# Kernel optimization log

Hardware: AMD Instinct MI355X
Metric: run time of the kernel (lower is better)

Reference implementation:

```python
import jax, jax.numpy as jnp
import numpy as np

ORB = 54          # unify_orb_num = 27 * 2
N_ATOMS = 64
N_EDGES = 1536
N_P = 256
N_Q = 384
F_P, F_Q, F_O = 0.0002, 0.0001, 0.00015


def setup_inputs() -> dict:
    key = jax.random.key(0)
    ks = jax.random.split(key, 16)
    M = ORB * N_ATOMS
    lattice_vector = 10.0 * jnp.eye(3, dtype=jnp.float32) + 0.1 * jax.random.normal(ks[0], (3, 3), jnp.float32)
    atoms_positions = 10.0 * jax.random.uniform(ks[1], (N_ATOMS, 3), jnp.float32)
    edge_src = jax.random.randint(ks[2], (N_EDGES,), 0, N_ATOMS, jnp.int32)
    edge_dst = jax.random.randint(ks[3], (N_EDGES,), 0, N_ATOMS, jnp.int32)
    # edge_vec = (pos_j - pos_i) + R @ lattice so that round(cell_inv @ R_dis) recovers integer R
    R_int = jax.random.randint(ks[4], (N_EDGES, 3), -2, 3).astype(jnp.float32)
    edge_vec = (atoms_positions[edge_dst] - atoms_positions[edge_src]) + R_int @ lattice_vector
    hr_gt = jax.random.normal(ks[5], (N_EDGES, ORB, ORB), jnp.float32)
    hr_pred = hr_gt + 0.1 * jax.random.normal(ks[6], (N_EDGES, ORB, ORB), jnp.float32)
    kpt_coord = jax.random.uniform(ks[7], (3,), jnp.float32)
    s = np.float32(1.0 / np.sqrt(M))
    P_re = s * jax.random.normal(ks[8], (N_P, M), jnp.float32)
    P_im = s * jax.random.normal(ks[9], (N_P, M), jnp.float32)
    Q_re = s * jax.random.normal(ks[10], (N_Q, M), jnp.float32)
    Q_im = s * jax.random.normal(ks[11], (N_Q, M), jnp.float32)
    H_gt = jax.random.normal(ks[12], (N_EDGES, ORB, ORB), jnp.float32)
    pred_H = H_gt + 0.1 * jax.random.normal(ks[13], (N_EDGES, ORB, ORB), jnp.float32)
    overlap = jax.random.normal(ks[14], (N_EDGES, ORB, ORB), jnp.float32)
    mask_tensor = jnp.ones((N_EDGES, ORB, ORB), jnp.float32)
    return dict(edge_vec=edge_vec, lattice_vector=lattice_vector, atoms_positions=atoms_positions,
                hr_gt=hr_gt, hr_pred=hr_pred, kpt_coord=kpt_coord,
                P_re=P_re, P_im=P_im, Q_re=Q_re, Q_im=Q_im,
                H_gt=H_gt, pred_H=pred_H, overlap=overlap, mask_tensor=mask_tensor,
                edge_src=edge_src, edge_dst=edge_dst)


def _forward(edge_vec, lattice_vector, atoms_positions, hr_gt, hr_pred, kpt_coord,
             P_re, P_im, Q_re, Q_im, H_gt, pred_H, overlap, mask_tensor,
             edge_src, edge_dst):
    M = ORB * atoms_positions.shape[0]
    # --- get_R_list (vectorized): R_tot = round(inv(L^T) @ (edge_vec - (pos_j - pos_i))) ---
    cell_inv = jnp.linalg.inv(lattice_vector.T)
    R_dis = edge_vec - (atoms_positions[edge_dst] - atoms_positions[edge_src])   # [E,3]
    R_tot = jnp.round(R_dis @ cell_inv.T)                                        # [E,3]
    # --- cal_wfc_hk_vectorized: phase factors + block scatter into dense hk ---
    phase = jnp.exp(2j * jnp.pi * (R_tot @ kpt_coord)).astype(jnp.complex64)     # [E]
    idx = jnp.arange(ORB)
    rows = edge_src[:, None, None].astype(jnp.int32) * ORB + idx[None, :, None]  # [E,ORB,1]
    cols = edge_dst[:, None, None].astype(jnp.int32) * ORB + idx[None, None, :]  # [E,1,ORB]
    flat = (rows * M + cols).reshape(-1)                                         # [E*ORB*ORB]

    def build_hk(hr):
        contrib = phase[:, None, None] * hr.astype(jnp.complex64)                # [E,ORB,ORB]
        return jnp.zeros((M * M,), jnp.complex64).at[flat].add(contrib.reshape(-1)).reshape(M, M)

    P = (P_re + 1j * P_im).astype(jnp.complex64)   # [N_P, M]
    Q = (Q_re + 1j * Q_im).astype(jnp.complex64)   # [N_Q, M]

    def project(hk):
        PcH = P.conj() @ hk                        # [N_P, M]
        QcH = Q.conj() @ hk                        # [N_Q, M]
        return PcH @ P.T, QcH @ Q.T, PcH @ Q.T     # [N_P,N_P], [N_Q,N_Q], [N_P,N_Q]

    rP1, rQ1, rPQ1 = project(build_hk(hr_gt))
    rP2, rQ2, rPQ2 = project(build_hk(hr_pred))

    # --- grep_min_mu ---
    f_R = 1.0 - F_P - F_Q - F_O
    N1 = jnp.sum(mask_tensor)
    N2 = N_P * N_P
    N3 = N_Q * N_Q
    N4 = N_P * N_Q
    n1 = f_R * jnp.sum((pred_H - H_gt) * overlap) / N1   # real inputs: real(sum(x*conj(s)))
    d1 = f_R * jnp.sum(overlap * overlap) / N1
    n2 = F_P * jnp.real(jnp.trace(rP2 - rP1)) / N2
    d2 = F_P / N_P
    n3 = F_Q * jnp.real(jnp.trace(rQ2 - rQ1)) / N3
    d3 = F_Q / N_Q
    mu = jax.lax.stop_gradient((n1 + n2 + n3) / (d1 + d2 + d3))  # torch float(mu) detaches

    # --- cal_loss: L1 terms (reduction='none' then sum) ---
    l1 = lambda a, b: jnp.abs(a - b)
    loss_hr = l1(H_gt + mu * overlap, pred_H).sum()
    eyeP = jnp.eye(N_P, dtype=jnp.float32)
    eyeQ = jnp.eye(N_Q, dtype=jnp.float32)
    loss_p = l1(jnp.real(rP1) + mu * eyeP, jnp.real(rP2)).sum() + l1(jnp.imag(rP1), jnp.imag(rP2)).sum()
    loss_q = l1(jnp.real(rQ1) + mu * eyeQ, jnp.real(rQ2)).sum() + l1(jnp.imag(rQ1), jnp.imag(rQ2)).sum()
    loss_pq = l1(jnp.real(rPQ1), jnp.real(rPQ2)).sum() + l1(jnp.imag(rPQ1), jnp.imag(rPQ2)).sum()
    return f_R * loss_hr / N1 + F_P * loss_p / N2 + F_Q * loss_q / N3 + F_O * loss_pq / N4


def reference(edge_vec, lattice_vector, atoms_positions, hr_gt, hr_pred, kpt_coord,
              P_re, P_im, Q_re, Q_im, H_gt, pred_H, overlap, mask_tensor,
              edge_src, edge_dst):
    return _forward(edge_vec, lattice_vector, atoms_positions, hr_gt, hr_pred, kpt_coord,
                    P_re, P_im, Q_re, Q_im, H_gt, pred_H, overlap, mask_tensor,
                    edge_src, edge_dst)
```

## Files before the change

### kernel.cpp

```cpp
#include <hip/hip_runtime.h>
#include <math.h>

#define E_N    1536
#define NATOMS 64
#define M_DIM  3456
#define NP     256
#define NQ     384
#define HRSZ   2916

#define W_FP 0.0002f
#define W_FQ 0.0001f
#define W_FO 0.00015f
#define W_FR (1.0f - W_FP - W_FQ - W_FO)

typedef __attribute__((ext_vector_type(8))) short short8;
typedef __attribute__((ext_vector_type(4))) float f32x4;

__device__ __forceinline__ unsigned pk_bf16(float a, float b) {
    unsigned r;
    asm volatile("v_cvt_pk_bf16_f32 %0, %1, %2" : "=v"(r) : "v"(a), "v"(b));
    return r;
}
__device__ __forceinline__ unsigned short f2bf(float x) {
    unsigned u = __builtin_bit_cast(unsigned, x);
    unsigned r = (u + 0x7fffu + ((u >> 16) & 1u)) >> 16;
    return (unsigned short)r;
}

__device__ __forceinline__ void gload_lds16(const void* g, void* l) {
    __builtin_amdgcn_global_load_lds(
        (const __attribute__((address_space(1))) unsigned int*)g,
        (__attribute__((address_space(3))) unsigned int*)l, 16, 0, 0);
}

__device__ __forceinline__ float blockSum(float v, float* sm) {
    v += __shfl_down(v, 32); v += __shfl_down(v, 16); v += __shfl_down(v, 8);
    v += __shfl_down(v, 4);  v += __shfl_down(v, 2);  v += __shfl_down(v, 1);
    __syncthreads();
    if ((threadIdx.x & 63) == 0) sm[threadIdx.x >> 6] = v;
    __syncthreads();
    float r = 0.0f;
    if (threadIdx.x == 0) {
        int nw = blockDim.x >> 6;
        for (int i = 0; i < nw; ++i) r += sm[i];
    }
    return r;
}

__global__ void k_phase(const float* __restrict__ edge_vec,
                        const float* __restrict__ lat,
                        const float* __restrict__ apos,
                        const float* __restrict__ kpt,
                        const int* __restrict__ esrc,
                        const int* __restrict__ edst,
                        float* __restrict__ ph_re, float* __restrict__ ph_im,
                        int* __restrict__ bcnt, int* __restrict__ blist) {
    int e = blockIdx.x * blockDim.x + threadIdx.x;
    if (e >= E_N) return;
    float a00 = lat[0], a01 = lat[3], a02 = lat[6];
    float a10 = lat[1], a11 = lat[4], a12 = lat[7];
    float a20 = lat[2], a21 = lat[5], a22 = lat[8];
    float c00 = a11*a22 - a12*a21;
    float c01 = a12*a20 - a10*a22;
    float c02 = a10*a21 - a11*a20;
    float det = a00*c00 + a01*c01 + a02*c02;
    float id  = 1.0f / det;
    float i00 = c00*id;
    float i01 = (a02*a21 - a01*a22)*id;
    float i02 = (a01*a12 - a02*a11)*id;
    float i10 = c01*id;
    float i11 = (a00*a22 - a02*a20)*id;
    float i12 = (a02*a10 - a00*a12)*id;
    float i20 = c02*id;
    float i21 = (a01*a20 - a00*a21)*id;
    float i22 = (a00*a11 - a01*a10)*id;
    int s = esrc[e], d = edst[e];
    float r0 = edge_vec[e*3+0] - (apos[d*3+0] - apos[s*3+0]);
    float r1 = edge_vec[e*3+1] - (apos[d*3+1] - apos[s*3+1]);
    float r2 = edge_vec[e*3+2] - (apos[d*3+2] - apos[s*3+2]);
    float t0 = roundf(i00*r0 + i01*r1 + i02*r2);
    float t1 = roundf(i10*r0 + i11*r1 + i12*r2);
    float t2 = roundf(i20*r0 + i21*r1 + i22*r2);
    float ph = t0*kpt[0] + t1*kpt[1] + t2*kpt[2];
    float ang = 6.28318530717958647692f * ph;
    ph_re[e] = cosf(ang);
    ph_im[e] = sinf(ang);
    int p = atomicAdd(&bcnt[s], 1);
    if (p < 128) blist[s*128 + p] = (e << 6) | d;
}

__global__ __launch_bounds__(256) void k_prep(
        const float4* __restrict__ P_re, const float4* __restrict__ P_im,
        const float4* __restrict__ Q_re, const float4* __restrict__ Q_im,
        ushort4* __restrict__ Prebf, ushort4* __restrict__ Pimbf,
        ushort4* __restrict__ Qrebf, ushort4* __restrict__ Qimbf) {
    const int NP4 = NP*M_DIM/4;
    const int NQ4 = NQ*M_DIM/4;
    const int TOT = 2*NP4 + 2*NQ4;
    int stride = gridDim.x * blockDim.x;
    for (int i = blockIdx.x*blockDim.x + threadIdx.x; i < TOT; i += stride) {
        float4 v; ushort4* dst; int o;
        if (i < NP4)              { v = P_re[i];            dst = Prebf; o = i; }
        else if (i < 2*NP4)       { o = i - NP4;   v = P_im[o]; dst = Pimbf; }
        else if (i < 2*NP4+NQ4)   { o = i - 2*NP4; v = Q_re[o]; dst = Qrebf; }
        else                      { o = i - 2*NP4 - NQ4; v = Q_im[o]; dst = Qimbf; }
        ushort4 u;
        u.x = f2bf(v.x); u.y = f2bf(v.y); u.z = f2bf(v.z); u.w = f2bf(v.w);
        dst[o] = u;
    }
}

__global__ __launch_bounds__(256) void k_hrd(
        const float* __restrict__ hr_gt, const float* __restrict__ hr_pred,
        unsigned* __restrict__ hrdG) {
    int idx = blockIdx.x*blockDim.x + threadIdx.x;
    int e = idx >> 11;
    int p = idx & 2047;
    int i = p >> 5, j2 = p & 31;
    float d0 = 0.0f, d1 = 0.0f;
    if (i < 54 && j2 < 27) {
        int o = e*HRSZ + i*54 + 2*j2;
        float2 g = *(const float2*)(hr_gt + o);
        float2 q = *(const float2*)(hr_pred + o);
        d0 = q.x - g.x; d1 = q.y - g.y;
    }
    hrdG[e*2048 + i*32 + (((j2>>2) ^ (i & 7))<<2) + (j2 & 3)] = pk_bf16(d0, d1);
}

__global__ __launch_bounds__(256) void k_pqpad(
        const ushort* __restrict__ Prebf, const ushort* __restrict__ Pimbf,
        const ushort* __restrict__ Qrebf, const ushort* __restrict__ Qimbf,
        unsigned* __restrict__ PpadR, unsigned* __restrict__ PpadI) {
    int idx = blockIdx.x*blockDim.x + threadIdx.x;
    int j2 = idx & 31;
    int r  = idx >> 5;
    int c  = r % 640;
    int dst = r / 640;
    unsigned vr = 0, vi = 0;
    if (j2 < 27) {
        const ushort* sre = (c < NP) ? (Prebf + (size_t)c*M_DIM) : (Qrebf + (size_t)(c-NP)*M_DIM);
        const ushort* sim = (c < NP) ? (Pimbf + (size_t)c*M_DIM) : (Qimbf + (size_t)(c-NP)*M_DIM);
        int o = dst*54 + 2*j2;
        vr = *(const unsigned*)(sre + o);
        vi = *(const unsigned*)(sim + o);
    }
    int loc = (dst*640 + c)*32 + (((j2>>2) ^ (c & 7))<<2) + (j2 & 3);
    PpadR[loc] = vr;
    PpadI[loc] = vi;
}

__global__ __launch_bounds__(256) void k_red1(const float4* __restrict__ Hg,
                                              const float4* __restrict__ Hp,
                                              const float4* __restrict__ ov,
                                              const float4* __restrict__ mk,
                                              float* __restrict__ acc) {
    const int N4 = E_N*HRSZ/4;
    int stride = gridDim.x * blockDim.x;
    float s0 = 0, s1 = 0, s2 = 0;
    for (int i = blockIdx.x*blockDim.x + threadIdx.x; i < N4; i += stride) {
        float4 hg = Hg[i], hp = Hp[i], o = ov[i], m = mk[i];
        s0 += (hp.x-hg.x)*o.x + (hp.y-hg.y)*o.y + (hp.z-hg.z)*o.z + (hp.w-hg.w)*o.w;
        s1 += o.x*o.x + o.y*o.y + o.z*o.z + o.w*o.w;
        s2 += m.x + m.y + m.z + m.w;
    }
    __shared__ float sm[8];
    float r0 = blockSum(s0, sm);
    float r1 = blockSum(s1, sm);
    float r2 = blockSum(s2, sm);
    if (threadIdx.x == 0) {
        atomicAdd(&acc[0], r0);
        atomicAdd(&acc[1], r1);
        atomicAdd(&acc[2], r2);
    }
}

__global__ __launch_bounds__(256) void k_bp(
        const unsigned* __restrict__ hrdG,
        const unsigned* __restrict__ PpadR, const unsigned* __restrict__ PpadI,
        const float* __restrict__ phre, const float* __restrict__ phim,
        const int* __restrict__ bcnt, const int* __restrict__ blist,
        ushort* __restrict__ BPTPre, ushort* __restrict__ BPTPim,
        ushort* __restrict__ BPTQre, ushort* __restrict__ BPTQim) {
    __shared__ ushort lds[3*4096];

    int tid = threadIdx.x;
    int a   = blockIdx.x / 10;
    int t   = blockIdx.x - a*10;
    ushort *Or, *Oi; int col0;
    if (t < 4) { Or = BPTPre; Oi = BPTPim; col0 = t*64; }
    else       { Or = BPTQre; Oi = BPTQim; col0 = (t-4)*64; }
    int gp0 = (0)*0 + t*64;

    int ne = bcnt[a]; if (ne > 128) ne = 128;
    const int* lst = blist + a*128;

    int w = tid >> 6, l = tid & 63;
    int wr0 = (w >> 1) * 32, wc0 = (w & 1) * 32;
    int lr = l & 15, kq = l >> 4, lk4 = (l >> 4) * 4;

    f32x4 accRe[2][2] = {}, accIm[2][2] = {};

    for (int n = 0; n < ne; ++n) {
        int v = lst[n];
        int ee = v >> 6, dst = v & 63;
        float phr = phre[ee], phi_ = phim[ee];
        const ushort* g0 = (const ushort*)(hrdG + (size_t)ee*2048);
        const ushort* g1 = (const ushort*)(PpadR + ((size_t)dst*640 + gp0)*32);
        const ushort* g2 = (const ushort*)(PpadI + ((size_t)dst*640 + gp0)*32);

        __syncthreads();
        #pragma unroll
        for (int j = 0; j < 6; ++j) {
            int jj = w + j*4;
            int arr = jj >> 3, ch = jj & 7;
            const ushort* gb = (arr == 0) ? g0 : (arr == 1) ? g1 : g2;
            gload_lds16(gb + ch*512 + l*8, (void*)(lds + arr*4096 + ch*512));
        }
        asm volatile("s_waitcnt vmcnt(0)" ::: "memory");
        __syncthreads();

        const ushort* A = lds;
        const ushort* BR = lds + 4096;
        const ushort* BI = lds + 8192;
        short8 a0[2], a1[2], br0[2], br1[2], bi0[2], bi1[2];
        #pragma unroll
        for (int mr = 0; mr < 2; ++mr) {
            int r = wr0 + mr*16 + lr;
            a0[mr] = *(const short8*)(A + r*64 + ((kq     ^ (r & 7))<<3));
            a1[mr] = *(const short8*)(A + r*64 + (((4+kq) ^ (r & 7))<<3));
        }
        #pragma unroll
        for (int nc = 0; nc < 2; ++nc) {
            int c = wc0 + nc*16 + lr;
            br0[nc] = *(const short8*)(BR + c*64 + ((kq     ^ (c & 7))<<3));
            br1[nc] = *(const short8*)(BR + c*64 + (((4+kq) ^ (c & 7))<<3));
            bi0[nc] = *(const short8*)(BI + c*64 + ((kq     ^ (c & 7))<<3));
            bi1[nc] = *(const short8*)(BI + c*64 + (((4+kq) ^ (c & 7))<<3));
        }
        f32x4 z = {0.0f, 0.0f, 0.0f, 0.0f};
        f32x4 t1[2][2], t2[2][2];
        #pragma unroll
        for (int mr = 0; mr < 2; ++mr)
            #pragma unroll
            for (int nc = 0; nc < 2; ++nc) {
                t1[mr][nc] = __builtin_amdgcn_mfma_f32_16x16x32_bf16(a0[mr], br0[nc], z, 0, 0, 0);
                t1[mr][nc] = __builtin_amdgcn_mfma_f32_16x16x32_bf16(a1[mr], br1[nc], t1[mr][nc], 0, 0, 0);
                t2[mr][nc] = __builtin_amdgcn_mfma_f32_16x16x32_bf16(a0[mr], bi0[nc], z, 0, 0, 0);
                t2[mr][nc] = __builtin_amdgcn_mfma_f32_16x16x32_bf16(a1[mr], bi1[nc], t2[mr][nc], 0, 0, 0);
            }
        #pragma unroll
        for (int mr = 0; mr < 2; ++mr)
            #pragma unroll
            for (int nc = 0; nc < 2; ++nc)
                #pragma unroll
                for (int q = 0; q < 4; ++q) {
                    accRe[mr][nc][q] += phr*t1[mr][nc][q] - phi_*t2[mr][nc][q];
                    accIm[mr][nc][q] += phr*t2[mr][nc][q] + phi_*t1[mr][nc][q];
                }
    }

    #pragma unroll
    for (int mr = 0; mr < 2; ++mr)
        #pragma unroll
        for (int nc = 0; nc < 2; ++nc) {
            int ib = wr0 + mr*16 + lk4;
            if (ib < 54) {
                int cg = col0 + wc0 + nc*16 + lr;
                size_t base = (size_t)cg*M_DIM + (size_t)a*54 + ib;
                *(unsigned*)(Or + base) = pk_bf16(accRe[mr][nc][0], accRe[mr][nc][1]);
                *(unsigned*)(Oi + base) = pk_bf16(accIm[mr][nc][0], accIm[mr][nc][1]);
                if (ib + 2 < 54) {
                    *(unsigned*)(Or + base + 2) = pk_bf16(accRe[mr][nc][2], accRe[mr][nc][3]);
                    *(unsigned*)(Oi + base + 2) = pk_bf16(accIm[mr][nc][2], accIm[mr][nc][3]);
                }
            }
        }
}

#define GPAD 40
__global__ __launch_bounds__(256) void k_gemm(
        const ushort* __restrict__ Prebf, const ushort* __restrict__ Pimbf,
        const ushort* __restrict__ Qrebf, const ushort* __restrict__ Qimbf,
        const ushort* __restrict__ BPTPre, const ushort* __restrict__ BPTPim,
        const ushort* __restrict__ BPTQre, const ushort* __restrict__ BPTQim,
        float* __restrict__ part) {
    __shared__ ushort Ar[64*GPAD], Ai[64*GPAD], Br_[64*GPAD], Bi_[64*GPAD];
    int tid = threadIdx.x;
    int bid = blockIdx.x;
    int t = bid / 6, ks = bid - t*6;
    const ushort *Ag, *Aig, *Bg, *Big; float *Cre, *Cim; int NC, r0, c0;
    if (t < 16) {
        Ag = Prebf; Aig = Pimbf; Bg = BPTPre; Big = BPTPim;
        NC = NP; r0 = (t & 3)*64; c0 = (t >> 2)*64;
        Cre = part + (size_t)ks*2*65536; Cim = Cre + 65536;
    } else if (t < 52) {
        int u = t - 16;
        Ag = Qrebf; Aig = Qimbf; Bg = BPTQre; Big = BPTQim;
        NC = NQ; r0 = (u % 6)*64; c0 = (u / 6)*64;
        Cre = part + 786432 + (size_t)ks*2*147456; Cim = Cre + 147456;
    } else {
        int u = t - 52;
        Ag = Prebf; Aig = Pimbf; Bg = BPTQre; Big = BPTQim;
        NC = NQ; r0 = (u & 3)*64; c0 = (u >> 2)*64;
        Cre = part + 786432 + 1769472 + (size_t)ks*2*98304; Cim = Cre + 98304;
    }
    int k0 = ks * 576;
    int srow = tid >> 2, skq = (tid & 3) * 8;
    int w = tid >> 6, l = tid & 63;
    int wr0 = (w >> 1)*32, wc0 = (w & 1)*32;
    int lr = l & 15, lk = (l >> 4)*8, lk4 = (l >> 4)*4;

    const ushort* pa  = Ag  + (size_t)(r0+srow)*M_DIM + k0 + skq;
    const ushort* pai = Aig + (size_t)(r0+srow)*M_DIM + k0 + skq;
    const ushort* pb  = Bg  + (size_t)(c0+srow)*M_DIM + k0 + skq;
    const ushort* pbi = Big + (size_t)(c0+srow)*M_DIM + k0 + skq;

    short8 ra = *(const short8*)pa, rai = *(const short8*)pai;
    short8 rb = *(const short8*)pb, rbi = *(const short8*)pbi;

    f32x4 aRe[2][2] = {}, aIA[2][2] = {}, aIB[2][2] = {};
    for (int s = 0; s < 18; ++s) {
        __syncthreads();
        *(short8*)(Ar  + srow*GPAD + skq) = ra;
        *(short8*)(Ai  + srow*GPAD + skq) = rai;
        *(short8*)(Br_ + srow*GPAD + skq) = rb;
        *(short8*)(Bi_ + srow*GPAD + skq) = rbi;
        __syncthreads();
        if (s < 17) {
            int o = (s+1)*32;
            ra  = *(const short8*)(pa  + o);
            rai = *(const short8*)(pai + o);
            rb  = *(const short8*)(pb  + o);
            rbi = *(const short8*)(pbi + o);
        }
        short8 fa[2], fn[2], fb[2], fi[2];
        #pragma unroll
        for (int mr = 0; mr < 2; ++mr) {
            int r = wr0 + mr*16 + lr;
            fa[mr] = *(const short8*)(Ar + r*GPAD + lk);
            fn[mr] = *(const short8*)(Ai + r*GPAD + lk);
        }
        #pragma unroll
        for (int nc = 0; nc < 2; ++nc) {
            int c = wc0 + nc*16 + lr;
            fb[nc] = *(const short8*)(Br_ + c*GPAD + lk);
            fi[nc] = *(const short8*)(Bi_ + c*GPAD + lk);
        }
        #pragma unroll
        for (int mr = 0; mr < 2; ++mr)
            #pragma unroll
            for (int nc = 0; nc < 2; ++nc) {
                aRe[mr][nc] = __builtin_amdgcn_mfma_f32_16x16x32_bf16(fa[mr], fb[nc], aRe[mr][nc], 0, 0, 0);
                aRe[mr][nc] = __builtin_amdgcn_mfma_f32_16x16x32_bf16(fn[mr], fi[nc], aRe[mr][nc], 0, 0, 0);
                aIA[mr][nc] = __builtin_amdgcn_mfma_f32_16x16x32_bf16(fa[mr], fi[nc], aIA[mr][nc], 0, 0, 0);
                aIB[mr][nc] = __builtin_amdgcn_mfma_f32_16x16x32_bf16(fn[mr], fb[nc], aIB[mr][nc], 0, 0, 0);
            }
    }
    #pragma unroll
    for (int mr = 0; mr < 2; ++mr)
        #pragma unroll
        for (int nc = 0; nc < 2; ++nc)
            #pragma unroll
            for (int rr = 0; rr < 4; ++rr) {
                int row = r0 + wr0 + mr*16 + lk4 + rr;
                int col = c0 + wc0 + nc*16 + lr;
                Cre[(size_t)row*NC + col] = aRe[mr][nc][rr];
                Cim[(size_t)row*NC + col] = aIA[mr][nc][rr] - aIB[mr][nc][rr];
            }
}

__global__ void k_mu(const float* __restrict__ part, float* __restrict__ acc) {
    int t = threadIdx.x;
    float v1 = 0.0f, v2 = 0.0f;
    if (t < NP) {
        #pragma unroll
        for (int ks = 0; ks < 6; ++ks) v1 += part[ks*131072 + t*(NP+1)];
    }
    if (t < NQ) {
        const float* q = part + 786432;
        #pragma unroll
        for (int ks = 0; ks < 6; ++ks) v2 += q[ks*294912 + t*(NQ+1)];
    }
    __shared__ float sm[8];
    float trP = blockSum(v1, sm);
    float trQ = blockSum(v2, sm);
    if (t == 0) {
        float N1 = acc[2];
        float n1 = W_FR * acc[0] / N1;
        float d1 = W_FR * acc[1] / N1;
        float n2 = W_FP * trP / (float)(NP*NP);
        float n3 = W_FQ * trQ / (float)(NQ*NQ);
        float d2 = W_FP / (float)NP;
        float d3 = W_FQ / (float)NQ;
        acc[3] = (n1 + n2 + n3) / (d1 + d2 + d3);
    }
}

__global__ __launch_bounds__(256) void k_loss_hr(const float4* __restrict__ Hg,
                                                 const float4* __restrict__ Hp,
                                                 const float4* __restrict__ ov,
                                                 float* __restrict__ acc) {
    const int N4 = E_N*HRSZ/4;
    float mu = acc[3];
    int stride = gridDim.x * blockDim.x;
    float s = 0;
    for (int i = blockIdx.x*blockDim.x + threadIdx.x; i < N4; i += stride) {
        float4 hg = Hg[i], hp = Hp[i], o = ov[i];
        s += fabsf(hg.x + mu*o.x - hp.x) + fabsf(hg.y + mu*o.y - hp.y)
           + fabsf(hg.z + mu*o.z - hp.z) + fabsf(hg.w + mu*o.w - hp.w);
    }
    __shared__ float sm[8];
    float r = blockSum(s, sm);
    if (threadIdx.x == 0) atomicAdd(&acc[4], r);
}

__global__ __launch_bounds__(256) void k_loss_mats(
        const float* __restrict__ part, float* __restrict__ acc) {
    const int NPP = NP*NP, NQQ = NQ*NQ, NPQ = NP*NQ;
    float mu = acc[3];
    float sP = 0, sQ = 0, sPQ = 0;
    int stride = gridDim.x * blockDim.x;
    for (int i = blockIdx.x*blockDim.x + threadIdx.x; i < NPP+NQQ+NPQ; i += stride) {
        if (i < NPP) {
            float sre = 0, sim = 0;
            #pragma unroll
            for (int ks = 0; ks < 6; ++ks) {
                sre += part[ks*131072 + i];
                sim += part[ks*131072 + 65536 + i];
            }
            int r = i >> 8, c = i & 255;
            float d = (r == c) ? mu : 0.0f;
            sP += fabsf(d - sre) + fabsf(sim);
        } else if (i < NPP+NQQ) {
            int j = i - NPP;
            const float* q = part + 786432;
            float sre = 0, sim = 0;
            #pragma unroll
            for (int ks = 0; ks < 6; ++ks) {
                sre += q[ks*294912 + j];
                sim += q[ks*294912 + 147456 + j];
            }
            int r = j / NQ, c = j - r*NQ;
            float d = (r == c) ? mu : 0.0f;
            sQ += fabsf(d - sre) + fabsf(sim);
        } else {
            int j = i - (NPP+NQQ);
            const float* pq = part + 786432 + 1769472;
            float sre = 0, sim = 0;
            #pragma unroll
            for (int ks = 0; ks < 6; ++ks) {
                sre += pq[ks*196608 + j];
                sim += pq[ks*196608 + 98304 + j];
            }
            sPQ += fabsf(sre) + fabsf(sim);
        }
    }
    __shared__ float sm[8];
    float a1 = blockSum(sP, sm);
    float a2 = blockSum(sQ, sm);
    float a3 = blockSum(sPQ, sm);
    if (threadIdx.x == 0) {
        atomicAdd(&acc[5], a1);
        atomicAdd(&acc[6], a2);
        atomicAdd(&acc[7], a3);
    }
}

__global__ void k_final(const float* __restrict__ acc, float* __restrict__ out) {
    if (threadIdx.x == 0 && blockIdx.x == 0) {
        float N1 = acc[2];
        out[0] = W_FR*acc[4]/N1
               + W_FP*acc[5]/(float)(NP*NP)
               + W_FQ*acc[6]/(float)(NQ*NQ)
               + W_FO*acc[7]/(float)(NP*NQ);
    }
}

extern "C" void kernel_launch(void* const* d_in, const int* in_sizes, int n_in,
                              void* d_out, int out_size, void* d_ws, size_t ws_size,
                              hipStream_t stream) {
    const float* edge_vec = (const float*)d_in[0];
    const float* lattice  = (const float*)d_in[1];
    const float* apos     = (const float*)d_in[2];
    const float* hr_gt    = (const float*)d_in[3];
    const float* hr_pred  = (const float*)d_in[4];
    const float* kpt      = (const float*)d_in[5];
    const float* P_re     = (const float*)d_in[6];
    const float* P_im     = (const float*)d_in[7];
    const float* Q_re     = (const float*)d_in[8];
    const float* Q_im     = (const float*)d_in[9];
    const float* H_gt     = (const float*)d_in[10];
    const float* pred_H   = (const float*)d_in[11];
    const float* overlap  = (const float*)d_in[12];
    const float* mask     = (const float*)d_in[13];
    const int*   esrc     = (const int*)d_in[14];
    const int*   edst     = (const int*)d_in[15];
    float* out = (float*)d_out;

    float* ws   = (float*)d_ws;
    float* acc  = ws;
    int*   bcnt = (int*)(ws + 16);
    int*   blist= (int*)(ws + 80);
    float* phre = ws + 8272;
    float* phim = phre + E_N;
    ushort* us  = (ushort*)(ws + 16384);
    ushort* Prebf  = us;
    ushort* Pimbf  = Prebf  + (size_t)NP*M_DIM;
    ushort* Qrebf  = Pimbf  + (size_t)NP*M_DIM;
    ushort* Qimbf  = Qrebf  + (size_t)NQ*M_DIM;
    ushort* BPTPre = Qimbf  + (size_t)NQ*M_DIM;
    ushort* BPTPim = BPTPre + (size_t)NP*M_DIM;
    ushort* BPTQre = BPTPim + (size_t)NP*M_DIM;
    ushort* BPTQim = BPTQre + (size_t)NQ*M_DIM;
    unsigned* PpadR = (unsigned*)(BPTQim + (size_t)NQ*M_DIM);
    unsigned* PpadI = PpadR + (size_t)64*640*32;
    unsigned* hrdG  = PpadI + (size_t)64*640*32;
    float* part = (float*)hrdG;

    hipMemsetAsync(ws, 0, 320, stream);

    k_phase<<<E_N/256, 256, 0, stream>>>(edge_vec, lattice, apos, kpt, esrc, edst,
                                         phre, phim, bcnt, blist);
    k_prep<<<1024, 256, 0, stream>>>((const float4*)P_re, (const float4*)P_im,
                                     (const float4*)Q_re, (const float4*)Q_im,
                                     (ushort4*)Prebf, (ushort4*)Pimbf,
                                     (ushort4*)Qrebf, (ushort4*)Qimbf);
    k_hrd<<<E_N*2048/256, 256, 0, stream>>>(hr_gt, hr_pred, hrdG);
    k_pqpad<<<64*640*32/256, 256, 0, stream>>>(Prebf, Pimbf, Qrebf, Qimbf, PpadR, PpadI);
    k_red1<<<1024, 256, 0, stream>>>((const float4*)H_gt, (const float4*)pred_H,
                                     (const float4*)overlap, (const float4*)mask, acc);
    k_bp<<<NATOMS*10, 256, 0, stream>>>(hrdG, PpadR, PpadI, phre, phim, bcnt, blist,
                                        BPTPre, BPTPim, BPTQre, BPTQim);
    k_gemm<<<456, 256, 0, stream>>>(Prebf, Pimbf, Qrebf, Qimbf,
                                    BPTPre, BPTPim, BPTQre, BPTQim, part);
    k_mu<<<1, 512, 0, stream>>>(part, acc);
    k_loss_hr<<<1024, 256, 0, stream>>>((const float4*)H_gt, (const float4*)pred_H,
                                        (const float4*)overlap, acc);
    k_loss_mats<<<256, 256, 0, stream>>>(part, acc);
    k_final<<<1, 1, 0, stream>>>(acc, out);
}
```

Measured before the change: 338.3 us.

## Fuse preprocessing kernels, double-buffer k_bp loads, merge loss kernels

Five preprocessing kernels (phase, bf16 prep, hr diff, P/Q padding, first reduction) are merged into one launch with block-range dispatch. The padding path now reads fp32 P/Q directly instead of waiting on the bf16 copies, and the stores are widened to uint4. k_bp stages its edge list and phases in LDS and double-buffers its global-to-LDS loads so the next edge's tiles arrive while the current one computes. The two loss kernels are merged into one launch. This cuts launch overhead and serialization between kernels, at the cost of more LDS per k_bp block and a larger, branchier fused kernel.

```diff
diff --git a/kernel.cpp b/kernel.cpp
--- a/kernel.cpp
+++ b/kernel.cpp
@@ -12,6 +12,15 @@
 #define W_FQ 0.0001f
 #define W_FO 0.00015f
 #define W_FR (1.0f - W_FP - W_FQ - W_FO)
+
+#define B_HRD  3072
+#define B_RED  1094
+#define B_PQ   1280
+#define B_PREP 1080
+#define B_PH   6
+#define B_TOT  (B_HRD + B_RED + B_PQ + B_PREP + B_PH)
+
+#define B_LHR  1094
 
 typedef __attribute__((ext_vector_type(8))) short short8;
 typedef __attribute__((ext_vector_type(4))) float f32x4;
@@ -47,130 +56,148 @@
     return r;
 }
 
-__global__ void k_phase(const float* __restrict__ edge_vec,
-                        const float* __restrict__ lat,
-                        const float* __restrict__ apos,
-                        const float* __restrict__ kpt,
-                        const int* __restrict__ esrc,
-                        const int* __restrict__ edst,
-                        float* __restrict__ ph_re, float* __restrict__ ph_im,
-                        int* __restrict__ bcnt, int* __restrict__ blist) {
-    int e = blockIdx.x * blockDim.x + threadIdx.x;
-    if (e >= E_N) return;
-    float a00 = lat[0], a01 = lat[3], a02 = lat[6];
-    float a10 = lat[1], a11 = lat[4], a12 = lat[7];
-    float a20 = lat[2], a21 = lat[5], a22 = lat[8];
-    float c00 = a11*a22 - a12*a21;
-    float c01 = a12*a20 - a10*a22;
-    float c02 = a10*a21 - a11*a20;
-    float det = a00*c00 + a01*c01 + a02*c02;
-    float id  = 1.0f / det;
-    float i00 = c00*id;
-    float i01 = (a02*a21 - a01*a22)*id;
-    float i02 = (a01*a12 - a02*a11)*id;
-    float i10 = c01*id;
-    float i11 = (a00*a22 - a02*a20)*id;
-    float i12 = (a02*a10 - a00*a12)*id;
-    float i20 = c02*id;
-    float i21 = (a01*a20 - a00*a21)*id;
-    float i22 = (a00*a11 - a01*a10)*id;
-    int s = esrc[e], d = edst[e];
-    float r0 = edge_vec[e*3+0] - (apos[d*3+0] - apos[s*3+0]);
-    float r1 = edge_vec[e*3+1] - (apos[d*3+1] - apos[s*3+1]);
-    float r2 = edge_vec[e*3+2] - (apos[d*3+2] - apos[s*3+2]);
-    float t0 = roundf(i00*r0 + i01*r1 + i02*r2);
-    float t1 = roundf(i10*r0 + i11*r1 + i12*r2);
-    float t2 = roundf(i20*r0 + i21*r1 + i22*r2);
-    float ph = t0*kpt[0] + t1*kpt[1] + t2*kpt[2];
-    float ang = 6.28318530717958647692f * ph;
-    ph_re[e] = cosf(ang);
-    ph_im[e] = sinf(ang);
-    int p = atomicAdd(&bcnt[s], 1);
-    if (p < 128) blist[s*128 + p] = (e << 6) | d;
-}
-
-__global__ __launch_bounds__(256) void k_prep(
-        const float4* __restrict__ P_re, const float4* __restrict__ P_im,
-        const float4* __restrict__ Q_re, const float4* __restrict__ Q_im,
+__global__ __launch_bounds__(256) void k_pre(
+        const float* __restrict__ edge_vec, const float* __restrict__ lat,
+        const float* __restrict__ apos, const float* __restrict__ kpt,
+        const int* __restrict__ esrc, const int* __restrict__ edst,
+        const float* __restrict__ hr_gt, const float* __restrict__ hr_pred,
+        const float* __restrict__ P_re, const float* __restrict__ P_im,
+        const float* __restrict__ Q_re, const float* __restrict__ Q_im,
+        const float4* __restrict__ Hg, const float4* __restrict__ Hp,
+        const float4* __restrict__ ov, const float4* __restrict__ mk,
+        float* __restrict__ phre, float* __restrict__ phim,
+        int* __restrict__ bcnt, int* __restrict__ blist,
+        unsigned* __restrict__ hrdG,
+        unsigned* __restrict__ PpadR, unsigned* __restrict__ PpadI,
         ushort4* __restrict__ Prebf, ushort4* __restrict__ Pimbf,
-        ushort4* __restrict__ Qrebf, ushort4* __restrict__ Qimbf) {
-    const int NP4 = NP*M_DIM/4;
-    const int NQ4 = NQ*M_DIM/4;
-    const int TOT = 2*NP4 + 2*NQ4;
-    int stride = gridDim.x * blockDim.x;
-    for (int i = blockIdx.x*blockDim.x + threadIdx.x; i < TOT; i += stride) {
-        float4 v; ushort4* dst; int o;
-        if (i < NP4)              { v = P_re[i];            dst = Prebf; o = i; }
-        else if (i < 2*NP4)       { o = i - NP4;   v = P_im[o]; dst = Pimbf; }
-        else if (i < 2*NP4+NQ4)   { o = i - 2*NP4; v = Q_re[o]; dst = Qrebf; }
-        else                      { o = i - 2*NP4 - NQ4; v = Q_im[o]; dst = Qimbf; }
-        ushort4 u;
-        u.x = f2bf(v.x); u.y = f2bf(v.y); u.z = f2bf(v.z); u.w = f2bf(v.w);
-        dst[o] = u;
-    }
-}
-
-__global__ __launch_bounds__(256) void k_hrd(
-        const float* __restrict__ hr_gt, const float* __restrict__ hr_pred,
-        unsigned* __restrict__ hrdG) {
-    int idx = blockIdx.x*blockDim.x + threadIdx.x;
-    int e = idx >> 11;
-    int p = idx & 2047;
-    int i = p >> 5, j2 = p & 31;
-    float d0 = 0.0f, d1 = 0.0f;
-    if (i < 54 && j2 < 27) {
-        int o = e*HRSZ + i*54 + 2*j2;
-        float2 g = *(const float2*)(hr_gt + o);
-        float2 q = *(const float2*)(hr_pred + o);
-        d0 = q.x - g.x; d1 = q.y - g.y;
-    }
-    hrdG[e*2048 + i*32 + (((j2>>2) ^ (i & 7))<<2) + (j2 & 3)] = pk_bf16(d0, d1);
-}
-
-__global__ __launch_bounds__(256) void k_pqpad(
-        const ushort* __restrict__ Prebf, const ushort* __restrict__ Pimbf,
-        const ushort* __restrict__ Qrebf, const ushort* __restrict__ Qimbf,
-        unsigned* __restrict__ PpadR, unsigned* __restrict__ PpadI) {
-    int idx = blockIdx.x*blockDim.x + threadIdx.x;
-    int j2 = idx & 31;
-    int r  = idx >> 5;
-    int c  = r % 640;
-    int dst = r / 640;
-    unsigned vr = 0, vi = 0;
-    if (j2 < 27) {
-        const ushort* sre = (c < NP) ? (Prebf + (size_t)c*M_DIM) : (Qrebf + (size_t)(c-NP)*M_DIM);
-        const ushort* sim = (c < NP) ? (Pimbf + (size_t)c*M_DIM) : (Qimbf + (size_t)(c-NP)*M_DIM);
-        int o = dst*54 + 2*j2;
-        vr = *(const unsigned*)(sre + o);
-        vi = *(const unsigned*)(sim + o);
-    }
-    int loc = (dst*640 + c)*32 + (((j2>>2) ^ (c & 7))<<2) + (j2 & 3);
-    PpadR[loc] = vr;
-    PpadI[loc] = vi;
-}
-
-__global__ __launch_bounds__(256) void k_red1(const float4* __restrict__ Hg,
-                                              const float4* __restrict__ Hp,
-                                              const float4* __restrict__ ov,
-                                              const float4* __restrict__ mk,
-                                              float* __restrict__ acc) {
-    const int N4 = E_N*HRSZ/4;
-    int stride = gridDim.x * blockDim.x;
-    float s0 = 0, s1 = 0, s2 = 0;
-    for (int i = blockIdx.x*blockDim.x + threadIdx.x; i < N4; i += stride) {
-        float4 hg = Hg[i], hp = Hp[i], o = ov[i], m = mk[i];
-        s0 += (hp.x-hg.x)*o.x + (hp.y-hg.y)*o.y + (hp.z-hg.z)*o.z + (hp.w-hg.w)*o.w;
-        s1 += o.x*o.x + o.y*o.y + o.z*o.z + o.w*o.w;
-        s2 += m.x + m.y + m.z + m.w;
-    }
+        ushort4* __restrict__ Qrebf, ushort4* __restrict__ Qimbf,
+        float* __restrict__ acc) {
     __shared__ float sm[8];
-    float r0 = blockSum(s0, sm);
-    float r1 = blockSum(s1, sm);
-    float r2 = blockSum(s2, sm);
-    if (threadIdx.x == 0) {
-        atomicAdd(&acc[0], r0);
-        atomicAdd(&acc[1], r1);
-        atomicAdd(&acc[2], r2);
+    int bid = blockIdx.x;
+    int tid = threadIdx.x;
+
+    if (bid < B_HRD) {
+        int idx = bid*256 + tid;
+        int e = idx >> 9;
+        int p = idx & 511;
+        int i = p >> 3, q = p & 7;
+        unsigned outv[4] = {0,0,0,0};
+        if (i < 54 && q < 7) {
+            const float* g = hr_gt  + (size_t)e*HRSZ + i*54;
+            const float* h = hr_pred + (size_t)e*HRSZ + i*54;
+            #pragma unroll
+            for (int u = 0; u < 4; ++u) {
+                int j2 = q*4 + u;
+                if (j2 < 27) {
+                    float2 gg = *(const float2*)(g + 2*j2);
+                    float2 hh = *(const float2*)(h + 2*j2);
+                    outv[u] = pk_bf16(hh.x - gg.x, hh.y - gg.y);
+                }
+            }
+        }
+        *(uint4*)(hrdG + (size_t)e*2048 + i*32 + ((q ^ (i & 7)) << 2)) =
+            make_uint4(outv[0], outv[1], outv[2], outv[3]);
+    } else if (bid < B_HRD + B_RED) {
+        const int N4 = E_N*HRSZ/4;
+        int base = (bid - B_HRD)*1024 + tid;
+        float4 hg[4], hp[4], o[4], m[4];
+        #pragma unroll
+        for (int u = 0; u < 4; ++u) {
+            int i = base + u*256;
+            if (i < N4) { hg[u]=Hg[i]; hp[u]=Hp[i]; o[u]=ov[i]; m[u]=mk[i]; }
+            else { hg[u]=float4{0,0,0,0}; hp[u]=hg[u]; o[u]=hg[u]; m[u]=hg[u]; }
+        }
+        float s0 = 0, s1 = 0, s2 = 0;
+        #pragma unroll
+        for (int u = 0; u < 4; ++u) {
+            s0 += (hp[u].x-hg[u].x)*o[u].x + (hp[u].y-hg[u].y)*o[u].y
+                + (hp[u].z-hg[u].z)*o[u].z + (hp[u].w-hg[u].w)*o[u].w;
+            s1 += o[u].x*o[u].x + o[u].y*o[u].y + o[u].z*o[u].z + o[u].w*o[u].w;
+            s2 += m[u].x + m[u].y + m[u].z + m[u].w;
+        }
+        float r0 = blockSum(s0, sm);
+        float r1 = blockSum(s1, sm);
+        float r2 = blockSum(s2, sm);
+        if (tid == 0) {
+            atomicAdd(&acc[0], r0);
+            atomicAdd(&acc[1], r1);
+            atomicAdd(&acc[2], r2);
+        }
+    } else if (bid < B_HRD + B_RED + B_PQ) {
+        int idx = (bid - B_HRD - B_RED)*256 + tid;
+        int q = idx & 7;
+        int r = idx >> 3;
+        int c = r % 640;
+        int dst = r / 640;
+        const float* sre = (c < NP) ? (P_re + (size_t)c*M_DIM) : (Q_re + (size_t)(c-NP)*M_DIM);
+        const float* sim = (c < NP) ? (P_im + (size_t)c*M_DIM) : (Q_im + (size_t)(c-NP)*M_DIM);
+        unsigned vr[4] = {0,0,0,0}, vi[4] = {0,0,0,0};
+        if (q < 7) {
+            #pragma unroll
+            for (int u = 0; u < 4; ++u) {
+                int j2 = q*4 + u;
+                if (j2 < 27) {
+                    int o = dst*54 + 2*j2;
+                    float2 fr = *(const float2*)(sre + o);
+                    float2 fi = *(const float2*)(sim + o);
+                    vr[u] = pk_bf16(fr.x, fr.y);
+                    vi[u] = pk_bf16(fi.x, fi.y);
+                }
+            }
+        }
+        int loc = (dst*640 + c)*32 + ((q ^ (c & 7)) << 2);
+        *(uint4*)(PpadR + loc) = make_uint4(vr[0], vr[1], vr[2], vr[3]);
+        *(uint4*)(PpadI + loc) = make_uint4(vi[0], vi[1], vi[2], vi[3]);
+    } else if (bid < B_HRD + B_RED + B_PQ + B_PREP) {
+        const int NP4 = NP*M_DIM/4;
+        const int NQ4 = NQ*M_DIM/4;
+        int base = (bid - B_HRD - B_RED - B_PQ)*1024 + tid;
+        #pragma unroll
+        for (int u = 0; u < 4; ++u) {
+            int i = base + u*256;
+            const float4* src; ushort4* dst; int o;
+            if (i < NP4)            { src = (const float4*)P_re; dst = Prebf; o = i; }
+            else if (i < 2*NP4)     { src = (const float4*)P_im; dst = Pimbf; o = i - NP4; }
+            else if (i < 2*NP4+NQ4) { src = (const float4*)Q_re; dst = Qrebf; o = i - 2*NP4; }
+            else                    { src = (const float4*)Q_im; dst = Qimbf; o = i - 2*NP4 - NQ4; }
+            float4 v = src[o];
+            ushort4 uu;
+            uu.x = f2bf(v.x); uu.y = f2bf(v.y); uu.z = f2bf(v.z); uu.w = f2bf(v.w);
+            dst[o] = uu;
+        }
+    } else {
+        int e = (bid - B_HRD - B_RED - B_PQ - B_PREP)*256 + tid;
+        if (e >= E_N) return;
+        float a00 = lat[0], a01 = lat[3], a02 = lat[6];
+        float a10 = lat[1], a11 = lat[4], a12 = lat[7];
+        float a20 = lat[2], a21 = lat[5], a22 = lat[8];
+        float c00 = a11*a22 - a12*a21;
+        float c01 = a12*a20 - a10*a22;
+        float c02 = a10*a21 - a11*a20;
+        float det = a00*c00 + a01*c01 + a02*c02;
+        float id  = 1.0f / det;
+        float i00 = c00*id;
+        float i01 = (a02*a21 - a01*a22)*id;
+        float i02 = (a01*a12 - a02*a11)*id;
+        float i10 = c01*id;
+        float i11 = (a00*a22 - a02*a20)*id;
+        float i12 = (a02*a10 - a00*a12)*id;
+        float i20 = c02*id;
+        float i21 = (a01*a20 - a00*a21)*id;
+        float i22 = (a00*a11 - a01*a10)*id;
+        int s = esrc[e], d = edst[e];
+        float r0 = edge_vec[e*3+0] - (apos[d*3+0] - apos[s*3+0]);
+        float r1 = edge_vec[e*3+1] - (apos[d*3+1] - apos[s*3+1]);
+        float r2 = edge_vec[e*3+2] - (apos[d*3+2] - apos[s*3+2]);
+        float t0 = roundf(i00*r0 + i01*r1 + i02*r2);
+        float t1 = roundf(i10*r0 + i11*r1 + i12*r2);
+        float t2 = roundf(i20*r0 + i21*r1 + i22*r2);
+        float ph = t0*kpt[0] + t1*kpt[1] + t2*kpt[2];
+        float ang = 6.28318530717958647692f * ph;
+        phre[e] = cosf(ang);
+        phim[e] = sinf(ang);
+        int p = atomicAdd(&bcnt[s], 1);
+        if (p < 128) blist[s*128 + p] = (e << 6) | d;
     }
 }
 
@@ -181,7 +208,9 @@
         const int* __restrict__ bcnt, const int* __restrict__ blist,
         ushort* __restrict__ BPTPre, ushort* __restrict__ BPTPim,
         ushort* __restrict__ BPTQre, ushort* __restrict__ BPTQim) {
-    __shared__ ushort lds[3*4096];
+    __shared__ ushort lds[2][12288];
+    __shared__ int elist[128];
+    __shared__ float phs[2][128];
 
     int tid = threadIdx.x;
     int a   = blockIdx.x / 10;
@@ -189,39 +218,52 @@
     ushort *Or, *Oi; int col0;
     if (t < 4) { Or = BPTPre; Oi = BPTPim; col0 = t*64; }
     else       { Or = BPTQre; Oi = BPTQim; col0 = (t-4)*64; }
-    int gp0 = (0)*0 + t*64;
 
     int ne = bcnt[a]; if (ne > 128) ne = 128;
-    const int* lst = blist + a*128;
+    for (int k = tid; k < ne; k += 256) {
+        int v = blist[a*128 + k];
+        elist[k] = v;
+        phs[0][k] = phre[v >> 6];
+        phs[1][k] = phim[v >> 6];
+    }
+    __syncthreads();
 
     int w = tid >> 6, l = tid & 63;
-    int wr0 = (w >> 1) * 32, wc0 = (w & 1) * 32;
-    int lr = l & 15, kq = l >> 4, lk4 = (l >> 4) * 4;
+    int wr0 = (w >> 1)*32, wc0 = (w & 1)*32;
+    int lr = l & 15, kq = l >> 4, lk4 = (l >> 4)*4;
 
     f32x4 accRe[2][2] = {}, accIm[2][2] = {};
 
+    #define ISSUE(nn, bb) do {                                                     \
+        int v_ = elist[(nn)];                                                      \
+        int ee_ = v_ >> 6, dst_ = v_ & 63;                                         \
+        const ushort* g0_ = (const ushort*)(hrdG + (size_t)ee_*2048);              \
+        const ushort* g1_ = (const ushort*)(PpadR + ((size_t)dst_*640 + t*64)*32); \
+        const ushort* g2_ = (const ushort*)(PpadI + ((size_t)dst_*640 + t*64)*32); \
+        ushort* lb_ = &lds[(bb)][0];                                               \
+        _Pragma("unroll")                                                          \
+        for (int j_ = 0; j_ < 6; ++j_) {                                           \
+            int jj_ = w + j_*4;                                                    \
+            int arr_ = jj_ >> 3, ch_ = jj_ & 7;                                    \
+            const ushort* gb_ = (arr_ == 0) ? g0_ : (arr_ == 1) ? g1_ : g2_;       \
+            gload_lds16(gb_ + ch_*512 + l*8, (void*)(lb_ + arr_*4096 + ch_*512));  \
+        }                                                                          \
+    } while (0)
+
+    if (ne > 0) ISSUE(0, 0);
     for (int n = 0; n < ne; ++n) {
-        int v = lst[n];
-        int ee = v >> 6, dst = v & 63;
-        float phr = phre[ee], phi_ = phim[ee];
-        const ushort* g0 = (const ushort*)(hrdG + (size_t)ee*2048);
-        const ushort* g1 = (const ushort*)(PpadR + ((size_t)dst*640 + gp0)*32);
-        const ushort* g2 = (const ushort*)(PpadI + ((size_t)dst*640 + gp0)*32);
-
+        int cur = n & 1;
+        if (n + 1 < ne) {
+            ISSUE(n+1, 1-cur);
+            asm volatile("s_waitcnt vmcnt(6)" ::: "memory");
+        } else {
+            asm volatile("s_waitcnt vmcnt(0)" ::: "memory");
+        }
         __syncthreads();
-        #pragma unroll
-        for (int j = 0; j < 6; ++j) {
-            int jj = w + j*4;
-            int arr = jj >> 3, ch = jj & 7;
-            const ushort* gb = (arr == 0) ? g0 : (arr == 1) ? g1 : g2;
-            gload_lds16(gb + ch*512 + l*8, (void*)(lds + arr*4096 + ch*512));
-        }
-        asm volatile("s_waitcnt vmcnt(0)" ::: "memory");
-        __syncthreads();
-
-        const ushort* A = lds;
-        const ushort* BR = lds + 4096;
-        const ushort* BI = lds + 8192;
+        float phr = phs[0][n], phi_ = phs[1][n];
+        const ushort* A  = &lds[cur][0];
+        const ushort* BR = A + 4096;
+        const ushort* BI = A + 8192;
         short8 a0[2], a1[2], br0[2], br1[2], bi0[2], bi1[2];
         #pragma unroll
         for (int mr = 0; mr < 2; ++mr) {
@@ -257,7 +299,9 @@
                     accRe[mr][nc][q] += phr*t1[mr][nc][q] - phi_*t2[mr][nc][q];
                     accIm[mr][nc][q] += phr*t2[mr][nc][q] + phi_*t1[mr][nc][q];
                 }
-    }
+        __syncthreads();
+    }
+    #undef ISSUE
 
     #pragma unroll
     for (int mr = 0; mr < 2; ++mr)
@@ -396,73 +440,79 @@
     }
 }
 
-__global__ __launch_bounds__(256) void k_loss_hr(const float4* __restrict__ Hg,
-                                                 const float4* __restrict__ Hp,
-                                                 const float4* __restrict__ ov,
-                                                 float* __restrict__ acc) {
-    const int N4 = E_N*HRSZ/4;
+__global__ __launch_bounds__(256) void k_loss(
+        const float4* __restrict__ Hg, const float4* __restrict__ Hp,
+        const float4* __restrict__ ov, const float* __restrict__ part,
+        float* __restrict__ acc) {
+    __shared__ float sm[8];
+    int bid = blockIdx.x;
+    int tid = threadIdx.x;
     float mu = acc[3];
-    int stride = gridDim.x * blockDim.x;
-    float s = 0;
-    for (int i = blockIdx.x*blockDim.x + threadIdx.x; i < N4; i += stride) {
-        float4 hg = Hg[i], hp = Hp[i], o = ov[i];
-        s += fabsf(hg.x + mu*o.x - hp.x) + fabsf(hg.y + mu*o.y - hp.y)
-           + fabsf(hg.z + mu*o.z - hp.z) + fabsf(hg.w + mu*o.w - hp.w);
-    }
-    __shared__ float sm[8];
-    float r = blockSum(s, sm);
-    if (threadIdx.x == 0) atomicAdd(&acc[4], r);
-}
-
-__global__ __launch_bounds__(256) void k_loss_mats(
-        const float* __restrict__ part, float* __restrict__ acc) {
-    const int NPP = NP*NP, NQQ = NQ*NQ, NPQ = NP*NQ;
-    float mu = acc[3];
-    float sP = 0, sQ = 0, sPQ = 0;
-    int stride = gridDim.x * blockDim.x;
-    for (int i = blockIdx.x*blockDim.x + threadIdx.x; i < NPP+NQQ+NPQ; i += stride) {
-        if (i < NPP) {
-            float sre = 0, sim = 0;
-            #pragma unroll
-            for (int ks = 0; ks < 6; ++ks) {
-                sre += part[ks*131072 + i];
-                sim += part[ks*131072 + 65536 + i];
-            }
-            int r = i >> 8, c = i & 255;
-            float d = (r == c) ? mu : 0.0f;
-            sP += fabsf(d - sre) + fabsf(sim);
-        } else if (i < NPP+NQQ) {
-            int j = i - NPP;
-            const float* q = part + 786432;
-            float sre = 0, sim = 0;
-            #pragma unroll
-            for (int ks = 0; ks < 6; ++ks) {
-                sre += q[ks*294912 + j];
-                sim += q[ks*294912 + 147456 + j];
-            }
-            int r = j / NQ, c = j - r*NQ;
-            float d = (r == c) ? mu : 0.0f;
-            sQ += fabsf(d - sre) + fabsf(sim);
-        } else {
-            int j = i - (NPP+NQQ);
-            const float* pq = part + 786432 + 1769472;
-            float sre = 0, sim = 0;
-            #pragma unroll
-            for (int ks = 0; ks < 6; ++ks) {
-                sre += pq[ks*196608 + j];
-                sim += pq[ks*196608 + 98304 + j];
-            }
-            sPQ += fabsf(sre) + fabsf(sim);
-        }
-    }
-    __shared__ float sm[8];
-    float a1 = blockSum(sP, sm);
-    float a2 = blockSum(sQ, sm);
-    float a3 = blockSum(sPQ, sm);
-    if (threadIdx.x == 0) {
-        atomicAdd(&acc[5], a1);
-        atomicAdd(&acc[6], a2);
-        atomicAdd(&acc[7], a3);
+    if (bid < B_LHR) {
+        const int N4 = E_N*HRSZ/4;
+        int base = bid*1024 + tid;
+        float4 hg[4], hp[4], o[4];
+        #pragma unroll
+        for (int u = 0; u < 4; ++u) {
+            int i = base + u*256;
+            if (i < N4) { hg[u]=Hg[i]; hp[u]=Hp[i]; o[u]=ov[i]; }
+            else { hg[u]=float4{0,0,0,0}; hp[u]=hg[u]; o[u]=hg[u]; }
+        }
+        float s = 0;
+        #pragma unroll
+        for (int u = 0; u < 4; ++u) {
+            s += fabsf(hg[u].x + mu*o[u].x - hp[u].x) + fabsf(hg[u].y + mu*o[u].y - hp[u].y)
+               + fabsf(hg[u].z + mu*o[u].z - hp[u].z) + fabsf(hg[u].w + mu*o[u].w - hp[u].w);
+        }
+        float r = blockSum(s, sm);
+        if (tid == 0) atomicAdd(&acc[4], r);
+    } else {
+        const int NPP = NP*NP, NQQ = NQ*NQ, NPQ = NP*NQ;
+        float sP = 0, sQ = 0, sPQ = 0;
+        int stride = 256*256;
+        for (int i = (bid - B_LHR)*256 + tid; i < NPP+NQQ+NPQ; i += stride) {
+            if (i < NPP) {
+                float sre = 0, sim = 0;
+                #pragma unroll
+                for (int ks = 0; ks < 6; ++ks) {
+                    sre += part[ks*131072 + i];
+                    sim += part[ks*131072 + 65536 + i];
+                }
+                int r = i >> 8, c = i & 255;
+                float d = (r == c) ? mu : 0.0f;
+                sP += fabsf(d - sre) + fabsf(sim);
+            } else if (i < NPP+NQQ) {
+                int j = i - NPP;
+                const float* q = part + 786432;
+                float sre = 0, sim = 0;
+                #pragma unroll
+                for (int ks = 0; ks < 6; ++ks) {
+                    sre += q[ks*294912 + j];
+                    sim += q[ks*294912 + 147456 + j];
+                }
+                int r = j / NQ, c = j - r*NQ;
+                float d = (r == c) ? mu : 0.0f;
+                sQ += fabsf(d - sre) + fabsf(sim);
+            } else {
+                int j = i - (NPP+NQQ);
+                const float* pq = part + 786432 + 1769472;
+                float sre = 0, sim = 0;
+                #pragma unroll
+                for (int ks = 0; ks < 6; ++ks) {
+                    sre += pq[ks*196608 + j];
+                    sim += pq[ks*196608 + 98304 + j];
+                }
+                sPQ += fabsf(sre) + fabsf(sim);
+            }
+        }
+        float a1 = blockSum(sP, sm);
+        float a2 = blockSum(sQ, sm);
+        float a3 = blockSum(sPQ, sm);
+        if (tid == 0) {
+            atomicAdd(&acc[5], a1);
+            atomicAdd(&acc[6], a2);
+            atomicAdd(&acc[7], a3);
+        }
     }
 }
 
@@ -519,23 +569,20 @@
 
     hipMemsetAsync(ws, 0, 320, stream);
 
-    k_phase<<<E_N/256, 256, 0, stream>>>(edge_vec, lattice, apos, kpt, esrc, edst,
-                                         phre, phim, bcnt, blist);
-    k_prep<<<1024, 256, 0, stream>>>((const float4*)P_re, (const float4*)P_im,
-                                     (const float4*)Q_re, (const float4*)Q_im,
+    k_pre<<<B_TOT, 256, 0, stream>>>(edge_vec, lattice, apos, kpt, esrc, edst,
+                                     hr_gt, hr_pred, P_re, P_im, Q_re, Q_im,
+                                     (const float4*)H_gt, (const float4*)pred_H,
+                                     (const float4*)overlap, (const float4*)mask,
+                                     phre, phim, bcnt, blist,
+                                     hrdG, PpadR, PpadI,
                                      (ushort4*)Prebf, (ushort4*)Pimbf,
-                                     (ushort4*)Qrebf, (ushort4*)Qimbf);
-    k_hrd<<<E_N*2048/256, 256, 0, stream>>>(hr_gt, hr_pred, hrdG);
-    k_pqpad<<<64*640*32/256, 256, 0, stream>>>(Prebf, Pimbf, Qrebf, Qimbf, PpadR, PpadI);
-    k_red1<<<1024, 256, 0, stream>>>((const float4*)H_gt, (const float4*)pred_H,
-                                     (const float4*)overlap, (const float4*)mask, acc);
+                                     (ushort4*)Qrebf, (ushort4*)Qimbf, acc);
     k_bp<<<NATOMS*10, 256, 0, stream>>>(hrdG, PpadR, PpadI, phre, phim, bcnt, blist,
                                         BPTPre, BPTPim, BPTQre, BPTQim);
     k_gemm<<<456, 256, 0, stream>>>(Prebf, Pimbf, Qrebf, Qimbf,
                                     BPTPre, BPTPim, BPTQre, BPTQim, part);
     k_mu<<<1, 512, 0, stream>>>(part, acc);
-    k_loss_hr<<<1024, 256, 0, stream>>>((const float4*)H_gt, (const float4*)pred_H,
-                                        (const float4*)overlap, acc);
-    k_loss_mats<<<256, 256, 0, stream>>>(part, acc);
+    k_loss<<<B_LHR + 256, 256, 0, stream>>>((const float4*)H_gt, (const float4*)pred_H,
+                                            (const float4*)overlap, part, acc);
     k_final<<<1, 1, 0, stream>>>(acc, out);
 }
```

Result: faster. 308.2 us (-8.9%).
